# Kernel tuning notes

Hardware: AMD Instinct MI355X
Metric: run time of the kernel (lower is better)

## Reference

```python
import jax, jax.numpy as jnp
import numpy as np

N = 50000      # nodes
E = 800000     # edges (avg degree 16)
DIN = 256      # input_dim
DH = 128       # hidden_dim
ALPHA_LOGIT = 0.6190392084062235  # logit(0.65)


def setup_inputs() -> dict:
    key = jax.random.key(0)
    ks = jax.random.split(key, 12)
    f = lambda k, s: jax.random.normal(k, s, dtype=jnp.float32)
    return {
        "x": f(ks[0], (N, DIN)),
        "edge_index": jax.random.randint(ks[1], (2, E), 0, N, dtype=jnp.int32),
        "reranker_scores": f(ks[2], (N,)),
        # input_proj
        "Wp": f(ks[3], (DIN, DH)) * 0.02, "bp": jnp.zeros((DH,), jnp.float32),
        # SAGEConv 0: lin_l (aggregated neighbors, with bias), lin_r (root, no bias)
        "Wl0": f(ks[4], (DIN, DH)) * 0.02, "bl0": jnp.zeros((DH,), jnp.float32),
        "Wr0": f(ks[5], (DIN, DH)) * 0.02,
        # SAGEConv 1
        "Wl1": f(ks[6], (DH, DH)) * 0.02, "bl1": jnp.zeros((DH,), jnp.float32),
        "Wr1": f(ks[7], (DH, DH)) * 0.02,
        # score head MLP
        "W1": f(ks[8], (DH, DH // 2)) * 0.02, "b1": jnp.zeros((DH // 2,), jnp.float32),
        "W2": f(ks[9], (DH // 2, 1)) * 0.02, "b2": jnp.zeros((1,), jnp.float32),
        "alpha_logit": jnp.float32(ALPHA_LOGIT),
    }


def _sage_conv(h, src, dst, Wl, bl, Wr):
    # PyG SAGEConv (aggr='mean', root_weight=True):
    # out = lin_l(mean_{j in N(i)} h_j) + lin_r(h_i)
    msg = h[src]                                             # [E, d] gather
    agg = jax.ops.segment_sum(msg, dst, num_segments=N)      # [N, d]
    cnt = jax.ops.segment_sum(jnp.ones((src.shape[0],), h.dtype), dst, num_segments=N)
    agg = agg / jnp.maximum(cnt, 1.0)[:, None]               # mean; isolated nodes -> 0
    return agg @ Wl + bl + h @ Wr


def reference(x, edge_index, reranker_scores, Wp, bp, Wl0, bl0, Wr0,
              Wl1, bl1, Wr1, W1, b1, W2, b2, alpha_logit):
    src, dst = edge_index[0], edge_index[1]
    # norm_type='none' -> no input normalization; eval mode -> dropout is identity
    residual = x @ Wp + bp                                   # [N, DH]
    h = jax.nn.relu(_sage_conv(x, src, dst, Wl0, bl0, Wr0)) + residual
    h = jax.nn.relu(_sage_conv(h, src, dst, Wl1, bl1, Wr1)) + h
    gnn_scores = (jax.nn.relu(h @ W1 + b1) @ W2 + b2)[:, 0]  # [N]
    alpha = jax.nn.sigmoid(alpha_logit)
    return alpha * reranker_scores + (1.0 - alpha) * gnn_scores
```

## Files before the change

### kernel.cpp

```cpp
#include <hip/hip_runtime.h>
#include <hip/hip_bf16.h>


#define DIN 256
#define DH 128
#define NPB 512
#define NBMAX 128
#define EPB 2048
#define JL (EPB/256)
#define CAP 12288
#define SLOTS 16384

typedef __attribute__((ext_vector_type(8))) short short8;
typedef __attribute__((ext_vector_type(4))) float float4v;
typedef __attribute__((ext_vector_type(2))) float float2v;

__device__ inline ushort f2b(float f){
  unsigned u = __float_as_uint(f);
  u = (u + 0x7fffu + ((u >> 16) & 1u)) >> 16;
  return (ushort)u;
}
__device__ inline float blo(unsigned v){ return __uint_as_float(v << 16); }
__device__ inline float bhi(unsigned v){ return __uint_as_float(v & 0xffff0000u); }
__device__ inline short8 pack8(float4 f0, float4 f1){
  short8 v;
  v[0]=(short)f2b(f0.x); v[1]=(short)f2b(f0.y); v[2]=(short)f2b(f0.z); v[3]=(short)f2b(f0.w);
  v[4]=(short)f2b(f1.x); v[5]=(short)f2b(f1.y); v[6]=(short)f2b(f1.z); v[7]=(short)f2b(f1.w);
  return v;
}
__device__ inline void glds16(const ushort* g, ushort* l){
  __builtin_amdgcn_global_load_lds((const __attribute__((address_space(1))) void*)g,
                                   (__attribute__((address_space(3))) void*)l, 16, 0, 0);
}
__device__ inline unsigned char enc8(float v){
  return (unsigned char)(__builtin_amdgcn_cvt_pk_fp8_f32(v, v, 0, false) & 0xFF);
}
__device__ inline float2v dec8(unsigned u){
  return __builtin_amdgcn_cvt_pk_f32_fp8((int)u, false);
}

__global__ __launch_bounds__(256) void fused_front(
    const float* __restrict__ x, int N, ushort* __restrict__ xb, int nstripe,
    const float* __restrict__ Wp, const float* __restrict__ Wl0, const float* __restrict__ Wr0,
    const float* __restrict__ Wl1, const float* __restrict__ Wr1, const float* __restrict__ W1,
    ushort* __restrict__ Wpf, ushort* __restrict__ Wl0f, ushort* __restrict__ Wr0f,
    ushort* __restrict__ Wl1f, ushort* __restrict__ Wr1f, ushort* __restrict__ W1f,
    const int* __restrict__ src, const int* __restrict__ dst, int E, int NB,
    int* __restrict__ bucketCnt, int* __restrict__ pairS, int* __restrict__ pairD,
    int nPart, int nConv)
{
  __shared__ int hist[NBMAX], lbase[NBMAX], gbase[NBMAX], lcur[NBMAX], sc[NBMAX];
  __shared__ int ls[EPB], ld[EPB];
  int bid = blockIdx.x;
  int t = threadIdx.x;

  if (bid < nPart){
    int base = bid * EPB;
    int cntE = E - base; if (cntE > EPB) cntE = EPB;
    for (int i=t;i<NB;i+=256) hist[i]=0;
    __syncthreads();
    int myS[JL], myD[JL];
    #pragma unroll
    for (int j=0;j<JL;j++){
      int e = base + j*256 + t;
      if (e < E){ myS[j]=src[e]; myD[j]=dst[e]; atomicAdd(&hist[myD[j]>>9],1); }
      else myD[j] = -1;
    }
    __syncthreads();
    if (t < NBMAX) sc[t] = (t < NB)? hist[t] : 0;
    __syncthreads();
    for (int st=1; st<NBMAX; st<<=1){
      int v = 0;
      if (t < NBMAX && t >= st) v = sc[t-st];
      __syncthreads();
      if (t < NBMAX) sc[t] += v;
      __syncthreads();
    }
    if (t < NB){
      int excl = (t>0)? sc[t-1] : 0;
      lbase[t] = excl; lcur[t] = excl;
      gbase[t] = atomicAdd(&bucketCnt[t], hist[t]);
    }
    __syncthreads();
    #pragma unroll
    for (int j=0;j<JL;j++){
      if (myD[j] >= 0){
        int b = myD[j] >> 9;
        int p = atomicAdd(&lcur[b], 1);
        ls[p] = myS[j]; ld[p] = myD[j];
      }
    }
    __syncthreads();
    for (int i=t;i<cntE;i+=256){
      int d = ld[i];
      int b = d >> 9;
      int p = gbase[b] + (i - lbase[b]);
      if (p < SLOTS){
        pairS[(size_t)b*SLOTS + p] = ls[i];
        pairD[(size_t)b*SLOTS + p] = d;
      }
    }
  } else if (bid < nPart + nConv){
    int gi = (bid - nPart)*256 + t;
    if (gi < nstripe*512){
      int L = gi & 63, ks = (gi>>6)&7, s = gi>>9;
      int row = s*16 + (L&15);
      int k = ks*32 + (L>>4)*8;
      short8 v;
      if (row < N){
        const float* p = x + (size_t)row*DIN + k;
        v = pack8(*(const float4*)p, *(const float4*)(p+4));
      } else {
        #pragma unroll
        for (int j=0;j<8;j++) v[j]=0;
      }
      *(short8*)(xb + (size_t)gi*8) = v;
    }
  } else {
    int gi = (bid - nPart - nConv)*256 + t;
    if (gi < 17408){
      const float* sw; ushort* dw; int cols, b0;
      if      (gi <  4096){ sw=Wp;  dw=Wpf;  cols=128; b0=0; }
      else if (gi <  8192){ sw=Wl0; dw=Wl0f; cols=128; b0=4096; }
      else if (gi < 12288){ sw=Wr0; dw=Wr0f; cols=128; b0=8192; }
      else if (gi < 14336){ sw=Wl1; dw=Wl1f; cols=128; b0=12288; }
      else if (gi < 16384){ sw=Wr1; dw=Wr1f; cols=128; b0=14336; }
      else                { sw=W1;  dw=W1f;  cols=64;  b0=16384; }
      int i = gi - b0;
      int ln = i & 63, g = i >> 6;
      int ntq = cols >> 4;
      int nt = g % ntq, ks = g / ntq;
      int col = nt*16 + (ln & 15);
      int k0 = ks*32 + (ln >> 4)*8;
      short8 v;
      #pragma unroll
      for (int j=0;j<8;j++) v[j] = (short)f2b(sw[(size_t)(k0+j)*cols + col]);
      *(short8*)(dw + (size_t)i*8) = v;
    }
  }
}

__global__ __launch_bounds__(256) void gemm0_csr(
    const ushort* __restrict__ xb, int N, int nstripe, int ngemm,
    const ushort* __restrict__ Wpf, const ushort* __restrict__ Wl0f, const ushort* __restrict__ Wr0f,
    const float* __restrict__ bp,
    ushort* __restrict__ xp, unsigned char* __restrict__ q8, ushort* __restrict__ xr0,
    const int* __restrict__ bucketCnt, const int* __restrict__ pairS, const int* __restrict__ pairD,
    int* __restrict__ off, int* __restrict__ deg, int* __restrict__ adj)
{
  __shared__ __align__(16) ushort smem[32768];
  int bid = blockIdx.x, t = threadIdx.x;

  if (bid < ngemm){
    int mat = bid % 3, b = bid / 3;
    int nblk = ngemm / 3;
    const ushort* Wf = (mat==0)? Wpf : (mat==1)? Wl0f : Wr0f;
    int w = t>>6, lane = t&63, lq = lane&15, quad = lane>>4;
    #pragma unroll
    for (int j=0;j<16;j++){
      int g = w + j*4;
      glds16(Wf + (size_t)g*512 + lane*8, smem + g*512);
    }
    __syncthreads();
    float bias[8];
    #pragma unroll
    for (int nt=0;nt<8;nt++) bias[nt] = (mat==0)? bp[nt*16 + lq] : 0.f;
    int nchunk = (nstripe + 3) >> 2;
    for (int c = b; c < nchunk; c += nblk){
      int stripe = c*4 + w;
      int row0 = stripe*16;
      if (row0 >= N) continue;
      short8 av[8];
      #pragma unroll
      for (int ks=0;ks<8;ks++)
        av[ks] = *(const short8*)(xb + ((size_t)stripe*8 + ks)*512 + lane*8);
      float4v acc[8];
      #pragma unroll
      for (int nt=0;nt<8;nt++)
        #pragma unroll
        for (int r=0;r<4;r++) acc[nt][r] = 0.f;
      #pragma unroll
      for (int ks=0;ks<8;ks++){
        #pragma unroll
        for (int nt=0;nt<8;nt++){
          short8 bf = *(const short8*)(smem + (size_t)((ks*8 + nt)*64 + lane)*8);
          acc[nt] = __builtin_amdgcn_mfma_f32_16x16x32_bf16(av[ks], bf, acc[nt], 0,0,0);
        }
      }
      if (mat == 1){
        #pragma unroll
        for (int nt=0;nt<8;nt++)
          #pragma unroll
          for (int r=0;r<4;r++){
            int row = row0 + quad*4 + r;
            if (row < N) q8[(size_t)row*128 + nt*16 + lq] = enc8(acc[nt][r]);
          }
      } else {
        ushort* Y = (mat==0)? xp : xr0;
        #pragma unroll
        for (int nt=0;nt<8;nt++)
          #pragma unroll
          for (int r=0;r<4;r++){
            int row = row0 + quad*4 + r;
            if (row < N) Y[(size_t)row*128 + nt*16 + lq] = f2b(acc[nt][r] + bias[nt]);
          }
      }
    }
  } else {
    int b = bid - ngemm;
    int* cnt  = (int*)smem;
    int* offl = cnt + NPB;
    int* s1   = offl + NPB + 1;
    int* win  = s1 + 256;
    int node0 = b * NPB;
    int base  = b * SLOTS;
    int ce = bucketCnt[b]; if (ce > SLOTS) ce = SLOTS;
    for (int i=t;i<NPB;i+=256) cnt[i]=0;
    __syncthreads();
    for (int i=t;i<ce;i+=256) atomicAdd(&cnt[pairD[(size_t)base+i]-node0], 1);
    __syncthreads();
    int a0 = cnt[2*t], a1 = cnt[2*t+1];
    s1[t] = a0 + a1;
    __syncthreads();
    for (int st=1; st<256; st<<=1){
      int v = (t>=st)? s1[t-st] : 0;
      __syncthreads();
      s1[t] += v;
      __syncthreads();
    }
    int excl = (t>0)? s1[t-1] : 0;
    offl[2*t] = excl; offl[2*t+1] = excl + a0;
    __syncthreads();
    for (int i=t;i<NPB;i+=256){
      int node = node0 + i;
      if (node < N){ off[node] = base + offl[i]; deg[node] = cnt[i]; }
    }
    __syncthreads();
    if (ce <= CAP){
      for (int i=t;i<ce;i+=256){
        int d = pairD[(size_t)base+i];
        int p = atomicAdd(&offl[d-node0], 1);
        win[p] = pairS[(size_t)base+i];
      }
      __syncthreads();
      for (int i=t;i<ce;i+=256) adj[(size_t)base+i] = win[i];
    } else {
      for (int i=t;i<ce;i+=256){
        int d = pairD[(size_t)base+i];
        int p = atomicAdd(&offl[d-node0], 1);
        adj[(size_t)base+p] = pairS[(size_t)base+i];
      }
    }
  }
}

__global__ __launch_bounds__(256) void combine0_f8(
    const unsigned char* __restrict__ agg8, const ushort* __restrict__ rootsrc,
    const ushort* __restrict__ ressrc, const float* __restrict__ bias,
    const int* __restrict__ off, const int* __restrict__ deg,
    const int* __restrict__ adj, ushort* __restrict__ out, int n)
{
  int t = threadIdx.x;
  int d = t & 63;
  int node = blockIdx.x*4 + (t >> 6);
  if (node >= n) return;
  int s = off[node], e = s + deg[node];
  const ushort* a8 = (const ushort*)agg8;
  float a0 = 0.f, a1 = 0.f;
  int p = s;
  for (; p+16 <= e; p += 16){
    ushort u[16];
    #pragma unroll
    for (int j=0;j<16;j++) u[j] = a8[(size_t)adj[p+j]*64 + d];
    #pragma unroll
    for (int j=0;j<16;j++){
      float2v f = dec8(u[j]);
      a0 += f[0]; a1 += f[1];
    }
  }
  for (; p+4 <= e; p += 4){
    ushort u0 = a8[(size_t)adj[p  ]*64 + d];
    ushort u1 = a8[(size_t)adj[p+1]*64 + d];
    ushort u2 = a8[(size_t)adj[p+2]*64 + d];
    ushort u3 = a8[(size_t)adj[p+3]*64 + d];
    float2v f0 = dec8(u0), f1 = dec8(u1), f2 = dec8(u2), f3 = dec8(u3);
    a0 += (f0[0]+f1[0]) + (f2[0]+f3[0]);
    a1 += (f0[1]+f1[1]) + (f2[1]+f3[1]);
  }
  for (; p < e; p++){
    float2v f = dec8(a8[(size_t)adj[p]*64 + d]);
    a0 += f[0]; a1 += f[1];
  }
  int cnt = e - s;
  float inv = 1.f / (float)((cnt > 1)? cnt : 1);
  unsigned rt = ((const unsigned*)rootsrc)[(size_t)node*64 + d];
  unsigned rs = ((const unsigned*)ressrc)[(size_t)node*64 + d];
  float o0 = fmaxf(a0*inv + bias[2*d]   + blo(rt), 0.f) + blo(rs);
  float o1 = fmaxf(a1*inv + bias[2*d+1] + bhi(rt), 0.f) + bhi(rs);
  ((unsigned*)out)[(size_t)node*64 + d] = (unsigned)f2b(o0) | ((unsigned)f2b(o1) << 16);
}

__global__ __launch_bounds__(256) void gemm1_wres(
    const ushort* __restrict__ h, int N,
    const ushort* __restrict__ Wl1f, const ushort* __restrict__ Wr1f,
    unsigned char* __restrict__ q8, ushort* __restrict__ hr1)
{
  __shared__ __align__(16) ushort Bs[32768];
  int t = threadIdx.x, w = t>>6, lane = t&63, lq = lane&15, quad = lane>>4;
  int tile = blockIdx.x;
  #pragma unroll
  for (int j=0;j<16;j++){
    int r = w + j*4;
    int m = r>>5, g = r&31;
    const ushort* Wm = m ? Wr1f : Wl1f;
    glds16(Wm + (size_t)g*512 + lane*8, Bs + r*512);
  }
  short8 av[2][4];
  int row0 = tile*128 + w*32;
  #pragma unroll
  for (int mt=0;mt<2;mt++){
    int row = row0 + mt*16 + lq; if (row >= N) row = N-1;
    #pragma unroll
    for (int ks=0;ks<4;ks++)
      av[mt][ks] = *(const short8*)(h + (size_t)row*128 + ks*32 + quad*8);
  }
  __syncthreads();
  #pragma unroll
  for (int m=0;m<2;m++){
    float4v acc[2][8];
    #pragma unroll
    for (int i=0;i<2;i++)
      #pragma unroll
      for (int j=0;j<8;j++)
        #pragma unroll
        for (int r=0;r<4;r++) acc[i][j][r] = 0.f;
    #pragma unroll
    for (int ks=0;ks<4;ks++){
      #pragma unroll
      for (int nt=0;nt<8;nt++){
        short8 bf = *(const short8*)(Bs + ((m*32 + ks*8 + nt)*64 + lane)*8);
        acc[0][nt] = __builtin_amdgcn_mfma_f32_16x16x32_bf16(av[0][ks], bf, acc[0][nt], 0,0,0);
        acc[1][nt] = __builtin_amdgcn_mfma_f32_16x16x32_bf16(av[1][ks], bf, acc[1][nt], 0,0,0);
      }
    }
    #pragma unroll
    for (int mt=0;mt<2;mt++){
      #pragma unroll
      for (int r=0;r<4;r++){
        int row = row0 + mt*16 + quad*4 + r;
        if (row < N){
          if (m == 0){
            #pragma unroll
            for (int nt=0;nt<8;nt++)
              q8[(size_t)row*128 + nt*16 + lq] = enc8(acc[mt][nt][r]);
          } else {
            #pragma unroll
            for (int nt=0;nt<8;nt++)
              hr1[(size_t)row*128 + nt*16 + lq] = f2b(acc[mt][nt][r]);
          }
        }
      }
    }
  }
}

__global__ __launch_bounds__(256) void combine1_head(
    const unsigned char* __restrict__ agg8, const ushort* __restrict__ hr1,
    const ushort* __restrict__ h, const float* __restrict__ bl1,
    const int* __restrict__ off, const int* __restrict__ deg, const int* __restrict__ adj,
    const ushort* __restrict__ W1f, const float* __restrict__ b1,
    const float* __restrict__ W2, const float* __restrict__ b2,
    const float* __restrict__ alogit, const float* __restrict__ rer,
    float* __restrict__ out, int n)
{
  __shared__ __align__(16) ushort W1s[8192];
  __shared__ __align__(16) ushort h2s[16*136];
  int t = threadIdx.x, w = t>>6, lane = t&63, lq = lane&15, quad = lane>>4;
  #pragma unroll
  for (int j=0;j<4;j++){
    int g = w + j*4;
    glds16(W1f + (size_t)g*512 + lane*8, W1s + g*512);
  }
  int node0 = blockIdx.x*16;
  unsigned* h2u = (unsigned*)h2s;
  const ushort* a8 = (const ushort*)agg8;
  #pragma unroll
  for (int j=0;j<4;j++){
    int node = node0 + w*4 + j;
    float o0 = 0.f, o1 = 0.f;
    if (node < n){
      int s = off[node], e = s + deg[node];
      float a0 = 0.f, a1 = 0.f;
      int p = s;
      for (; p+16 <= e; p += 16){
        ushort u[16];
        #pragma unroll
        for (int jj=0;jj<16;jj++) u[jj] = a8[(size_t)adj[p+jj]*64 + lane];
        #pragma unroll
        for (int jj=0;jj<16;jj++){
          float2v f = dec8(u[jj]);
          a0 += f[0]; a1 += f[1];
        }
      }
      for (; p+4 <= e; p += 4){
        ushort u0 = a8[(size_t)adj[p  ]*64 + lane];
        ushort u1 = a8[(size_t)adj[p+1]*64 + lane];
        ushort u2 = a8[(size_t)adj[p+2]*64 + lane];
        ushort u3 = a8[(size_t)adj[p+3]*64 + lane];
        float2v f0 = dec8(u0), f1 = dec8(u1), f2 = dec8(u2), f3 = dec8(u3);
        a0 += (f0[0]+f1[0]) + (f2[0]+f3[0]);
        a1 += (f0[1]+f1[1]) + (f2[1]+f3[1]);
      }
      for (; p < e; p++){
        float2v f = dec8(a8[(size_t)adj[p]*64 + lane]);
        a0 += f[0]; a1 += f[1];
      }
      int cnt = e - s;
      float inv = 1.f / (float)((cnt > 1)? cnt : 1);
      unsigned rt = ((const unsigned*)hr1)[(size_t)node*64 + lane];
      unsigned rs = ((const unsigned*)h)[(size_t)node*64 + lane];
      o0 = fmaxf(a0*inv + bl1[2*lane]   + blo(rt), 0.f) + blo(rs);
      o1 = fmaxf(a1*inv + bl1[2*lane+1] + bhi(rt), 0.f) + bhi(rs);
    }
    h2u[(w*4+j)*68 + lane] = (unsigned)f2b(o0) | ((unsigned)f2b(o1) << 16);
  }
  __syncthreads();

  short8 av[4];
  #pragma unroll
  for (int ks=0;ks<4;ks++)
    av[ks] = *(const short8*)(h2s + lq*136 + ks*32 + quad*8);
  float4v acc[4];
  #pragma unroll
  for (int nt=0;nt<4;nt++)
    #pragma unroll
    for (int r=0;r<4;r++) acc[nt][r] = 0.f;
  #pragma unroll
  for (int ks=0;ks<4;ks++){
    #pragma unroll
    for (int nt=0;nt<4;nt++){
      short8 bf = *(const short8*)(W1s + ((ks*4 + nt)*64 + lane)*8);
      acc[nt] = __builtin_amdgcn_mfma_f32_16x16x32_bf16(av[ks], bf, acc[nt], 0,0,0);
    }
  }
  float al = alogit[0];
  float a  = 1.f / (1.f + __expf(-al));
  float pw[4] = {0.f,0.f,0.f,0.f};
  #pragma unroll
  for (int nt=0; nt<4; nt++){
    int c = nt*16 + lq;
    float w2 = W2[c];
    float bb = b1[c];
    #pragma unroll
    for (int r=0; r<4; r++)
      pw[r] += fmaxf(acc[nt][r] + bb, 0.f) * w2;
  }
  #pragma unroll
  for (int mask=1; mask<16; mask<<=1){
    #pragma unroll
    for (int r=0; r<4; r++)
      pw[r] += __shfl_xor(pw[r], mask);
  }
  if (lq == 0){
    #pragma unroll
    for (int r=0; r<4; r++){
      int rl = quad*4 + r;
      if ((rl >> 2) == w){
        int node = node0 + rl;
        if (node < n)
          out[node] = a * rer[node] + (1.f - a) * (pw[r] + b2[0]);
      }
    }
  }
}

extern "C" void kernel_launch(void* const* d_in, const int* in_sizes, int n_in,
                              void* d_out, int out_size, void* d_ws, size_t ws_size,
                              hipStream_t stream)
{
  (void)n_in; (void)out_size; (void)ws_size;
  const float* x    = (const float*)d_in[0];
  const int*   ei   = (const int*)d_in[1];
  const float* rer  = (const float*)d_in[2];
  const float* Wp   = (const float*)d_in[3];
  const float* bp   = (const float*)d_in[4];
  const float* Wl0  = (const float*)d_in[5];
  const float* bl0  = (const float*)d_in[6];
  const float* Wr0  = (const float*)d_in[7];
  const float* Wl1  = (const float*)d_in[8];
  const float* bl1  = (const float*)d_in[9];
  const float* Wr1  = (const float*)d_in[10];
  const float* W1   = (const float*)d_in[11];
  const float* b1   = (const float*)d_in[12];
  const float* W2   = (const float*)d_in[13];
  const float* b2   = (const float*)d_in[14];
  const float* alogit = (const float*)d_in[15];

  const int N = in_sizes[2];
  const int E = in_sizes[1] / 2;
  const int* src = ei;
  const int* dst = ei + E;
  const int NB = (N + NPB - 1) / NPB;
  const int nstripe = (N + 15) / 16;
  const int ntile = (N + 127) / 128;
  const int nPart = (E + EPB - 1) / EPB;
  const int nConv = (nstripe*512 + 255)/256;

  ushort* U = (ushort*)d_ws;
  ushort* xb  = U;
  ushort* xp  = xb + (size_t)nstripe*512*8;
  ushort* xr0 = xp  + (size_t)N*DH;
  ushort* h   = xr0 + (size_t)N*DH;
  unsigned char* q8 = (unsigned char*)(h + (size_t)N*DH);
  ushort* Wpf  = (ushort*)(q8 + (size_t)N*DH);
  ushort* Wl0f = Wpf  + (size_t)4096*8;
  ushort* Wr0f = Wl0f + (size_t)4096*8;
  ushort* Wl1f = Wr0f + (size_t)4096*8;
  ushort* Wr1f = Wl1f + (size_t)2048*8;
  ushort* W1f  = Wr1f + (size_t)2048*8;
  int* I = (int*)(W1f + (size_t)1024*8);
  int* bucketCnt = I;
  int* off   = bucketCnt + NBMAX;
  int* deg   = off + N;
  int* pairS = deg + N;
  int* pairD = pairS + (size_t)NB*SLOTS;
  int* adj   = pairD + (size_t)NB*SLOTS;

  hipMemsetAsync(bucketCnt, 0, NBMAX*sizeof(int), stream);

  fused_front<<<nPart + nConv + 68, 256, 0, stream>>>(
      x, N, xb, nstripe, Wp, Wl0, Wr0, Wl1, Wr1, W1,
      Wpf, Wl0f, Wr0f, Wl1f, Wr1f, W1f,
      src, dst, E, NB, bucketCnt, pairS, pairD, nPart, nConv);

  gemm0_csr<<<768 + NB, 256, 0, stream>>>(
      xb, N, nstripe, 768, Wpf, Wl0f, Wr0f, bp, xp, q8, xr0,
      bucketCnt, pairS, pairD, off, deg, adj);

  combine0_f8<<<(N+3)/4, 256, 0, stream>>>(q8, xr0, xp, bl0, off, deg, adj, h, N);

  gemm1_wres<<<ntile, 256, 0, stream>>>(h, N, Wl1f, Wr1f, q8, xr0);

  combine1_head<<<(N+15)/16, 256, 0, stream>>>(
      q8, xr0, h, bl1, off, deg, adj, W1f, b1, W2, b2, alogit, rer, (float*)d_out, N);
}
```

Baseline: 258.6 us.

## Stage block adjacency in LDS and interleave four nodes' gathers per wave

Measured after the change: 385.7 us. 49.1% more time.

```diff
diff --git a/kernel.cpp b/kernel.cpp
--- a/kernel.cpp
+++ b/kernel.cpp
@@ -260,44 +260,183 @@
     const int* __restrict__ off, const int* __restrict__ deg,
     const int* __restrict__ adj, ushort* __restrict__ out, int n)
 {
-  int t = threadIdx.x;
-  int d = t & 63;
-  int node = blockIdx.x*4 + (t >> 6);
-  if (node >= n) return;
-  int s = off[node], e = s + deg[node];
+  __shared__ int adjl[1024];
+  int t = threadIdx.x, w = t>>6, lane = t&63;
+  int node0 = blockIdx.x*16;
+  int nlast = node0+15 < n-1 ? node0+15 : n-1;
+  int e0 = off[node0];
+  int eTot = off[nlast] + deg[nlast] - e0;
+  bool ovf = (eTot > 1024);
+  if (!ovf){
+    for (int i=t; i<eTot; i+=256) adjl[i] = adj[e0+i];
+  }
+  __syncthreads();
+  const int* ap = ovf ? (adj + e0) : (const int*)adjl;
   const ushort* a8 = (const ushort*)agg8;
-  float a0 = 0.f, a1 = 0.f;
-  int p = s;
-  for (; p+16 <= e; p += 16){
-    ushort u[16];
-    #pragma unroll
-    for (int j=0;j<16;j++) u[j] = a8[(size_t)adj[p+j]*64 + d];
-    #pragma unroll
-    for (int j=0;j<16;j++){
-      float2v f = dec8(u[j]);
-      a0 += f[0]; a1 += f[1];
-    }
-  }
-  for (; p+4 <= e; p += 4){
-    ushort u0 = a8[(size_t)adj[p  ]*64 + d];
-    ushort u1 = a8[(size_t)adj[p+1]*64 + d];
-    ushort u2 = a8[(size_t)adj[p+2]*64 + d];
-    ushort u3 = a8[(size_t)adj[p+3]*64 + d];
-    float2v f0 = dec8(u0), f1 = dec8(u1), f2 = dec8(u2), f3 = dec8(u3);
-    a0 += (f0[0]+f1[0]) + (f2[0]+f3[0]);
-    a1 += (f0[1]+f1[1]) + (f2[1]+f3[1]);
-  }
-  for (; p < e; p++){
-    float2v f = dec8(a8[(size_t)adj[p]*64 + d]);
-    a0 += f[0]; a1 += f[1];
-  }
-  int cnt = e - s;
-  float inv = 1.f / (float)((cnt > 1)? cnt : 1);
-  unsigned rt = ((const unsigned*)rootsrc)[(size_t)node*64 + d];
-  unsigned rs = ((const unsigned*)ressrc)[(size_t)node*64 + d];
-  float o0 = fmaxf(a0*inv + bias[2*d]   + blo(rt), 0.f) + blo(rs);
-  float o1 = fmaxf(a1*inv + bias[2*d+1] + bhi(rt), 0.f) + bhi(rs);
-  ((unsigned*)out)[(size_t)node*64 + d] = (unsigned)f2b(o0) | ((unsigned)f2b(o1) << 16);
+
+  int sl[4], dgv[4];
+  float a0[4] = {0.f,0.f,0.f,0.f}, a1[4] = {0.f,0.f,0.f,0.f};
+  int maxd = 0;
+  #pragma unroll
+  for (int j=0;j<4;j++){
+    int node = node0 + w*4 + j;
+    bool ok = node < n;
+    sl[j]  = ok ? off[node] - e0 : 0;
+    dgv[j] = ok ? deg[node] : 0;
+    if (dgv[j] > maxd) maxd = dgv[j];
+  }
+  for (int c=0; c<maxd; c+=16){
+    ushort u[4][16];
+    #pragma unroll
+    for (int j=0;j<4;j++){
+      int lim = dgv[j] - c;
+      #pragma unroll
+      for (int jj=0;jj<16;jj++)
+        if (jj < lim) u[j][jj] = a8[(size_t)ap[sl[j]+c+jj]*64 + lane];
+    }
+    #pragma unroll
+    for (int j=0;j<4;j++){
+      int lim = dgv[j] - c;
+      #pragma unroll
+      for (int jj=0;jj<16;jj++)
+        if (jj < lim){ float2v f = dec8(u[j][jj]); a0[j] += f[0]; a1[j] += f[1]; }
+    }
+  }
+  #pragma unroll
+  for (int j=0;j<4;j++){
+    int node = node0 + w*4 + j;
+    if (node >= n) continue;
+    int cnt = dgv[j];
+    float inv = 1.f / (float)((cnt > 1)? cnt : 1);
+    unsigned rt = ((const unsigned*)rootsrc)[(size_t)node*64 + lane];
+    unsigned rs = ((const unsigned*)ressrc)[(size_t)node*64 + lane];
+    float o0 = fmaxf(a0[j]*inv + bias[2*lane]   + blo(rt), 0.f) + blo(rs);
+    float o1 = fmaxf(a1[j]*inv + bias[2*lane+1] + bhi(rt), 0.f) + bhi(rs);
+    ((unsigned*)out)[(size_t)node*64 + lane] = (unsigned)f2b(o0) | ((unsigned)f2b(o1) << 16);
+  }
+}
+
+__global__ __launch_bounds__(256) void combine1_head(
+    const unsigned char* __restrict__ agg8, const ushort* __restrict__ hr1,
+    const ushort* __restrict__ h, const float* __restrict__ bl1,
+    const int* __restrict__ off, const int* __restrict__ deg, const int* __restrict__ adj,
+    const ushort* __restrict__ W1f, const float* __restrict__ b1,
+    const float* __restrict__ W2, const float* __restrict__ b2,
+    const float* __restrict__ alogit, const float* __restrict__ rer,
+    float* __restrict__ out, int n)
+{
+  __shared__ __align__(16) ushort W1s[8192];
+  __shared__ __align__(16) ushort h2s[16*136];
+  __shared__ int adjl[1024];
+  int t = threadIdx.x, w = t>>6, lane = t&63, lq = lane&15, quad = lane>>4;
+  #pragma unroll
+  for (int j=0;j<4;j++){
+    int g = w + j*4;
+    glds16(W1f + (size_t)g*512 + lane*8, W1s + g*512);
+  }
+  int node0 = blockIdx.x*16;
+  int nlast = node0+15 < n-1 ? node0+15 : n-1;
+  int e0 = off[node0];
+  int eTot = off[nlast] + deg[nlast] - e0;
+  bool ovf = (eTot > 1024);
+  if (!ovf){
+    for (int i=t; i<eTot; i+=256) adjl[i] = adj[e0+i];
+  }
+  __syncthreads();
+  const int* ap = ovf ? (adj + e0) : (const int*)adjl;
+  const ushort* a8 = (const ushort*)agg8;
+  unsigned* h2u = (unsigned*)h2s;
+
+  int sl[4], dgv[4];
+  float a0[4] = {0.f,0.f,0.f,0.f}, a1[4] = {0.f,0.f,0.f,0.f};
+  int maxd = 0;
+  #pragma unroll
+  for (int j=0;j<4;j++){
+    int node = node0 + w*4 + j;
+    bool ok = node < n;
+    sl[j]  = ok ? off[node] - e0 : 0;
+    dgv[j] = ok ? deg[node] : 0;
+    if (dgv[j] > maxd) maxd = dgv[j];
+  }
+  for (int c=0; c<maxd; c+=16){
+    ushort u[4][16];
+    #pragma unroll
+    for (int j=0;j<4;j++){
+      int lim = dgv[j] - c;
+      #pragma unroll
+      for (int jj=0;jj<16;jj++)
+        if (jj < lim) u[j][jj] = a8[(size_t)ap[sl[j]+c+jj]*64 + lane];
+    }
+    #pragma unroll
+    for (int j=0;j<4;j++){
+      int lim = dgv[j] - c;
+      #pragma unroll
+      for (int jj=0;jj<16;jj++)
+        if (jj < lim){ float2v f = dec8(u[j][jj]); a0[j] += f[0]; a1[j] += f[1]; }
+    }
+  }
+  #pragma unroll
+  for (int j=0;j<4;j++){
+    int node = node0 + w*4 + j;
+    float o0 = 0.f, o1 = 0.f;
+    if (node < n){
+      int cnt = dgv[j];
+      float inv = 1.f / (float)((cnt > 1)? cnt : 1);
+      unsigned rt = ((const unsigned*)hr1)[(size_t)node*64 + lane];
+      unsigned rs = ((const unsigned*)h)[(size_t)node*64 + lane];
+      o0 = fmaxf(a0[j]*inv + bl1[2*lane]   + blo(rt), 0.f) + blo(rs);
+      o1 = fmaxf(a1[j]*inv + bl1[2*lane+1] + bhi(rt), 0.f) + bhi(rs);
+    }
+    h2u[(w*4+j)*68 + lane] = (unsigned)f2b(o0) | ((unsigned)f2b(o1) << 16);
+  }
+  __syncthreads();
+
+  short8 av[4];
+  #pragma unroll
+  for (int ks=0;ks<4;ks++)
+    av[ks] = *(const short8*)(h2s + lq*136 + ks*32 + quad*8);
+  float4v acc[4];
+  #pragma unroll
+  for (int nt=0;nt<4;nt++)
+    #pragma unroll
+    for (int r=0;r<4;r++) acc[nt][r] = 0.f;
+  #pragma unroll
+  for (int ks=0;ks<4;ks++){
+    #pragma unroll
+    for (int nt=0;nt<4;nt++){
+      short8 bf = *(const short8*)(W1s + ((ks*4 + nt)*64 + lane)*8);
+      acc[nt] = __builtin_amdgcn_mfma_f32_16x16x32_bf16(av[ks], bf, acc[nt], 0,0,0);
+    }
+  }
+  float al = alogit[0];
+  float a  = 1.f / (1.f + __expf(-al));
+  float pw[4] = {0.f,0.f,0.f,0.f};
+  #pragma unroll
+  for (int nt=0; nt<4; nt++){
+    int c = nt*16 + lq;
+    float w2 = W2[c];
+    float bb = b1[c];
+    #pragma unroll
+    for (int r=0; r<4; r++)
+      pw[r] += fmaxf(acc[nt][r] + bb, 0.f) * w2;
+  }
+  #pragma unroll
+  for (int mask=1; mask<16; mask<<=1){
+    #pragma unroll
+    for (int r=0; r<4; r++)
+      pw[r] += __shfl_xor(pw[r], mask);
+  }
+  if (lq == 0){
+    #pragma unroll
+    for (int r=0; r<4; r++){
+      int rl = quad*4 + r;
+      if ((rl >> 2) == w){
+        int node = node0 + rl;
+        if (node < n)
+          out[node] = a * rer[node] + (1.f - a) * (pw[r] + b2[0]);
+      }
+    }
+  }
 }
 
 __global__ __launch_bounds__(256) void gemm1_wres(
@@ -359,116 +498,6 @@
               hr1[(size_t)row*128 + nt*16 + lq] = f2b(acc[mt][nt][r]);
           }
         }
-      }
-    }
-  }
-}
-
-__global__ __launch_bounds__(256) void combine1_head(
-    const unsigned char* __restrict__ agg8, const ushort* __restrict__ hr1,
-    const ushort* __restrict__ h, const float* __restrict__ bl1,
-    const int* __restrict__ off, const int* __restrict__ deg, const int* __restrict__ adj,
-    const ushort* __restrict__ W1f, const float* __restrict__ b1,
-    const float* __restrict__ W2, const float* __restrict__ b2,
-    const float* __restrict__ alogit, const float* __restrict__ rer,
-    float* __restrict__ out, int n)
-{
-  __shared__ __align__(16) ushort W1s[8192];
-  __shared__ __align__(16) ushort h2s[16*136];
-  int t = threadIdx.x, w = t>>6, lane = t&63, lq = lane&15, quad = lane>>4;
-  #pragma unroll
-  for (int j=0;j<4;j++){
-    int g = w + j*4;
-    glds16(W1f + (size_t)g*512 + lane*8, W1s + g*512);
-  }
-  int node0 = blockIdx.x*16;
-  unsigned* h2u = (unsigned*)h2s;
-  const ushort* a8 = (const ushort*)agg8;
-  #pragma unroll
-  for (int j=0;j<4;j++){
-    int node = node0 + w*4 + j;
-    float o0 = 0.f, o1 = 0.f;
-    if (node < n){
-      int s = off[node], e = s + deg[node];
-      float a0 = 0.f, a1 = 0.f;
-      int p = s;
-      for (; p+16 <= e; p += 16){
-        ushort u[16];
-        #pragma unroll
-        for (int jj=0;jj<16;jj++) u[jj] = a8[(size_t)adj[p+jj]*64 + lane];
-        #pragma unroll
-        for (int jj=0;jj<16;jj++){
-          float2v f = dec8(u[jj]);
-          a0 += f[0]; a1 += f[1];
-        }
-      }
-      for (; p+4 <= e; p += 4){
-        ushort u0 = a8[(size_t)adj[p  ]*64 + lane];
-        ushort u1 = a8[(size_t)adj[p+1]*64 + lane];
-        ushort u2 = a8[(size_t)adj[p+2]*64 + lane];
-        ushort u3 = a8[(size_t)adj[p+3]*64 + lane];
-        float2v f0 = dec8(u0), f1 = dec8(u1), f2 = dec8(u2), f3 = dec8(u3);
-        a0 += (f0[0]+f1[0]) + (f2[0]+f3[0]);
-        a1 += (f0[1]+f1[1]) + (f2[1]+f3[1]);
-      }
-      for (; p < e; p++){
-        float2v f = dec8(a8[(size_t)adj[p]*64 + lane]);
-        a0 += f[0]; a1 += f[1];
-      }
-      int cnt = e - s;
-      float inv = 1.f / (float)((cnt > 1)? cnt : 1);
-      unsigned rt = ((const unsigned*)hr1)[(size_t)node*64 + lane];
-      unsigned rs = ((const unsigned*)h)[(size_t)node*64 + lane];
-      o0 = fmaxf(a0*inv + bl1[2*lane]   + blo(rt), 0.f) + blo(rs);
-      o1 = fmaxf(a1*inv + bl1[2*lane+1] + bhi(rt), 0.f) + bhi(rs);
-    }
-    h2u[(w*4+j)*68 + lane] = (unsigned)f2b(o0) | ((unsigned)f2b(o1) << 16);
-  }
-  __syncthreads();
-
-  short8 av[4];
-  #pragma unroll
-  for (int ks=0;ks<4;ks++)
-    av[ks] = *(const short8*)(h2s + lq*136 + ks*32 + quad*8);
-  float4v acc[4];
-  #pragma unroll
-  for (int nt=0;nt<4;nt++)
-    #pragma unroll
-    for (int r=0;r<4;r++) acc[nt][r] = 0.f;
-  #pragma unroll
-  for (int ks=0;ks<4;ks++){
-    #pragma unroll
-    for (int nt=0;nt<4;nt++){
-      short8 bf = *(const short8*)(W1s + ((ks*4 + nt)*64 + lane)*8);
-      acc[nt] = __builtin_amdgcn_mfma_f32_16x16x32_bf16(av[ks], bf, acc[nt], 0,0,0);
-    }
-  }
-  float al = alogit[0];
-  float a  = 1.f / (1.f + __expf(-al));
-  float pw[4] = {0.f,0.f,0.f,0.f};
-  #pragma unroll
-  for (int nt=0; nt<4; nt++){
-    int c = nt*16 + lq;
-    float w2 = W2[c];
-    float bb = b1[c];
-    #pragma unroll
-    for (int r=0; r<4; r++)
-      pw[r] += fmaxf(acc[nt][r] + bb, 0.f) * w2;
-  }
-  #pragma unroll
-  for (int mask=1; mask<16; mask<<=1){
-    #pragma unroll
-    for (int r=0; r<4; r++)
-      pw[r] += __shfl_xor(pw[r], mask);
-  }
-  if (lq == 0){
-    #pragma unroll
-    for (int r=0; r<4; r++){
-      int rl = quad*4 + r;
-      if ((rl >> 2) == w){
-        int node = node0 + rl;
-        if (node < n)
-          out[node] = a * rer[node] + (1.f - a) * (pw[r] + b2[0]);
       }
     }
   }
@@ -537,7 +566,7 @@
       xb, N, nstripe, 768, Wpf, Wl0f, Wr0f, bp, xp, q8, xr0,
       bucketCnt, pairS, pairD, off, deg, adj);
 
-  combine0_f8<<<(N+3)/4, 256, 0, stream>>>(q8, xr0, xp, bl0, off, deg, adj, h, N);
+  combine0_f8<<<(N+15)/16, 256, 0, stream>>>(q8, xr0, xp, bl0, off, deg, adj, h, N);
 
   gemm1_wres<<<ntile, 256, 0, stream>>>(h, N, Wl1f, Wr1f, q8, xr0);
 
```
